# Kernel optimization log

Hardware: AMD Instinct MI355X
Metric: run time of the kernel (lower is better)

Reference implementation:

```python
import jax, jax.numpy as jnp
import numpy as np

D_MODEL = 512
DQ = D_MODEL // 4  # 128
TIME_SHIFT_START = 256
VELOCITY_START = 768
NOTE_OFF_START = 128


def conv1d(x, w, b, stride, pad):
    # x: [B, Cin, L], w: [Cout, Cin, K]
    y = jax.lax.conv_general_dilated(x, w, (stride,), [(pad, pad)],
                                     dimension_numbers=('NCH', 'OIH', 'NCH'))
    return y + b[None, :, None]


def adaptive_avg_pool1d(x, out_size):
    # faithful to torch AdaptiveAvgPool1d bin boundaries
    L = x.shape[-1]
    starts = (np.arange(out_size) * L) // out_size
    ends = np.ceil((np.arange(out_size) + 1) * L / out_size).astype(np.int64)
    cs = jnp.concatenate([jnp.zeros(x.shape[:-1] + (1,), x.dtype),
                          jnp.cumsum(x, axis=-1)], axis=-1)
    return (cs[..., ends] - cs[..., starts]) / jnp.asarray(ends - starts, x.dtype)


def setup_inputs() -> dict:
    key = jax.random.key(0)
    ks = jax.random.split(key, 20)

    def w(k, shape):
        fan_in = int(np.prod(shape[1:]))
        return jax.random.normal(k, shape, jnp.float32) / np.sqrt(fan_in)

    def b(k, n):
        return jax.random.normal(k, (n,), jnp.float32) * 0.01

    return {
        'tokens': jax.random.randint(ks[0], (32, 4096), 0, 774),
        'r1_w': w(ks[1], (32, 1, 8)),    'r1_b': b(ks[2], 32),
        'r2_w': w(ks[3], (64, 32, 4)),   'r2_b': b(ks[4], 64),
        'h1_w': w(ks[5], (64, 128, 12)), 'h1_b': b(ks[6], 64),
        'h2_w': w(ks[7], (32, 64, 8)),   'h2_b': b(ks[8], 32),
        'm1_w': w(ks[9], (64, 128, 5)),  'm1_b': b(ks[10], 64),
        'm2_w': w(ks[11], (32, 64, 3)),  'm2_b': b(ks[12], 32),
        'd1_w': w(ks[13], (16, 6, 4)),   'd1_b': b(ks[14], 16),
        'd2_w': w(ks[15], (16, 16, 3)),  'd2_b': b(ks[16], 16),
        'fc_w': w(ks[17], (D_MODEL, D_MODEL)), 'fc_b': b(ks[18], D_MODEL),
    }


def reference(tokens, r1_w, r1_b, r2_w, r2_b, h1_w, h1_b, h2_w, h2_b,
              m1_w, m1_b, m2_w, m2_b, d1_w, d1_b, d2_w, d2_b, fc_w, fc_b):
    B, S = tokens.shape
    relu = jax.nn.relu

    # rhythm: binary time-shift indicator [B,1,S]
    ts = ((tokens >= TIME_SHIFT_START) & (tokens < VELOCITY_START)).astype(jnp.float32)[:, None, :]
    r = relu(conv1d(ts, r1_w, r1_b, 2, 3))
    r = relu(conv1d(r, r2_w, r2_b, 2, 1))
    r = adaptive_avg_pool1d(r, DQ).reshape(B, -1)  # [B, 64*DQ]

    # vectorized one-hot pitch scatter (replaces the python double loop): [B,128,S]
    nm = tokens < NOTE_OFF_START
    pitch = jnp.transpose(
        jax.nn.one_hot(jnp.where(nm, tokens, 0) % 128, 128, dtype=jnp.float32)
        * nm[..., None].astype(jnp.float32), (0, 2, 1))

    h = relu(conv1d(pitch, h1_w, h1_b, 1, 6))
    h = relu(conv1d(h, h2_w, h2_b, 2, 3))
    h = adaptive_avg_pool1d(h, DQ).reshape(B, -1)  # [B, 32*DQ]

    m = relu(conv1d(pitch, m1_w, m1_b, 1, 2))
    m = relu(conv1d(m, m2_w, m2_b, 1, 1))
    m = adaptive_avg_pool1d(m, DQ).reshape(B, -1)  # [B, 32*DQ]

    # velocity one-hot scatter: [B,6,S]
    vm = tokens >= VELOCITY_START
    vel = jnp.clip(jnp.where(vm, tokens - VELOCITY_START, 0), 0, 5)
    vpat = jnp.transpose(
        jax.nn.one_hot(vel, 6, dtype=jnp.float32) * vm[..., None].astype(jnp.float32),
        (0, 2, 1))
    d = relu(conv1d(vpat, d1_w, d1_b, 1, 2))
    d = relu(conv1d(d, d2_w, d2_b, 1, 1))
    d = adaptive_avg_pool1d(d, DQ).reshape(B, -1)  # [B, 16*DQ]

    # total flattened size is 36*d_model != d_model, so torch branch always pools
    r, h, m, d = [adaptive_avg_pool1d(f[:, None, :], DQ)[:, 0] for f in (r, h, m, d)]

    combined = jnp.concatenate([r, h, m, d], axis=1)       # [B, d_model]
    feats = combined @ fc_w.T + fc_b                        # Linear
    return jnp.broadcast_to(feats[:, None, :], (B, S, D_MODEL))
```

## Files before the change

### kernel.cpp

```cpp
#include <hip/hip_runtime.h>

typedef unsigned short u16;
typedef unsigned int u32;
typedef float vf4 __attribute__((ext_vector_type(4)));
typedef unsigned int vu4 __attribute__((ext_vector_type(4)));
typedef short sh8 __attribute__((ext_vector_type(8)));
typedef float f32x4 __attribute__((ext_vector_type(4)));

__device__ __forceinline__ float bf2f(u16 u) {
  return __uint_as_float(((u32)u) << 16);
}
__device__ __forceinline__ u16 f2bf(float f) {
  u32 x = __float_as_uint(f);
  return (u16)((x + 0x7fffu + ((x >> 16) & 1u)) >> 16);
}
__device__ __forceinline__ float ldin(const void* p, int idx, int isf) {
  return isf ? ((const float*)p)[idx] : bf2f(((const u16*)p)[idx]);
}

#define OFF_FLAG  ((size_t)0)
#define OFF_WB    ((size_t)16)
#define OFF_WTH1  ((size_t)1180432)
#define OFF_WTM1  ((size_t)1573648)
#define OFF_COMB  ((size_t)1737488)
#define OFF_FEATF ((size_t)1803024)
#define OFF_FEATB ((size_t)1868560)
#define OFF_R1    ((size_t)1901328)
#define OFF_D1    ((size_t)10289936)
#define OFF_DP    ((size_t)18686736)
#define OFF_H1    ((size_t)18948880)
#define OFF_M1    ((size_t)35758864)
#define OFF_WH2B  ((size_t)52536080)
#define OFF_WH2L  ((size_t)52568848)
#define OFF_WM2B  ((size_t)52601616)
#define OFF_WM2L  ((size_t)52613904)
#define WS_NEEDED ((size_t)52626192)

#define WB_R1W 0
#define WB_R1B 256
#define WB_R2W 288
#define WB_R2B 8480
#define WB_H1B 8544
#define WB_H2W 8608
#define WB_H2B 24992
#define WB_M1B 25024
#define WB_M2W 25088
#define WB_M2B 31232
#define WB_D1W 31264
#define WB_D1B 31648
#define WB_D2W 31664
#define WB_D2B 32432
#define WB_FCW 32448
#define WB_FCB 294592
#define WB_TOTAL 295104

#define H1_STRIDE 4104
#define D1_STRIDE 4100

__global__ __launch_bounds__(256) void k_convert(
    const void* r1_w, const void* r1_b, const void* r2_w, const void* r2_b,
    const void* h1_w, const void* h1_b, const void* h2_w, const void* h2_b,
    const void* m1_w, const void* m1_b, const void* m2_w, const void* m2_b,
    const void* d1_w, const void* d1_b, const void* d2_w, const void* d2_b,
    const void* fc_w, const void* fc_b,
    int* __restrict__ flagp, float* __restrict__ wb,
    float* __restrict__ wTh1, float* __restrict__ wTm1,
    float* __restrict__ combined,
    u16* __restrict__ wh2b, u16* __restrict__ wh2l,
    u16* __restrict__ wm2b, u16* __restrict__ wm2l) {
  __shared__ int cnt[4];
  int tid = threadIdx.x;
  {
    u16 v = ((const u16*)fc_w)[2 * tid];
    int e = (v >> 7) & 0xFF;
    int outside = (e < 100 || e > 140) ? 1 : 0;
    unsigned long long m = __ballot(outside);
    if ((tid & 63) == 0) cnt[tid >> 6] = __popcll(m);
  }
  __syncthreads();
  int isf = (cnt[0] + cnt[1] + cnt[2] + cnt[3] >= 64) ? 1 : 0;
  if (blockIdx.x == 0 && tid == 0) flagp[0] = isf;

  int j = blockIdx.x * 256 + tid;
  if (j >= 473280) return;
  if (j < WB_TOTAL) {
    const void* src; int si;
    if      (j < WB_R1B) { src = r1_w; si = j; }
    else if (j < WB_R2W) { src = r1_b; si = j - WB_R1B; }
    else if (j < WB_R2B) { src = r2_w; si = j - WB_R2W; }
    else if (j < WB_H1B) { src = r2_b; si = j - WB_R2B; }
    else if (j < WB_H2W) { src = h1_b; si = j - WB_H1B; }
    else if (j < WB_H2B) { src = h2_w; si = j - WB_H2W; }
    else if (j < WB_M1B) { src = h2_b; si = j - WB_H2B; }
    else if (j < WB_M2W) { src = m1_b; si = j - WB_M1B; }
    else if (j < WB_M2B) { src = m2_w; si = j - WB_M2W; }
    else if (j < WB_D1W) { src = m2_b; si = j - WB_M2B; }
    else if (j < WB_D1B) { src = d1_w; si = j - WB_D1W; }
    else if (j < WB_D2W) { src = d1_b; si = j - WB_D1B; }
    else if (j < WB_D2B) { src = d2_w; si = j - WB_D2W; }
    else if (j < WB_FCW) { src = d2_b; si = j - WB_D2B; }
    else if (j < WB_FCB) { src = fc_w; si = j - WB_FCW; }
    else                 { src = fc_b; si = j - WB_FCB; }
    wb[j] = ldin(src, si, isf);
  } else if (j < 393408) {
    int j2 = j - WB_TOTAL;
    int o = j2 & 63, r = j2 >> 6, k = r % 12, p = r / 12;
    wTh1[j2] = ldin(h1_w, (o * 128 + p) * 12 + k, isf);
  } else if (j < 434368) {
    int j3 = j - 393408;
    int o = j3 & 63, r = j3 >> 6, k = r % 5, p = r / 5;
    wTm1[j3] = ldin(m1_w, (o * 128 + p) * 5 + k, isf);
  } else if (j < 450752) {
    combined[j - 434368] = 0.f;
  } else if (j < 467136) {
    int jj = j - 450752;
    int o = jj >> 9, rem = jj & 511, c = rem >> 3, kk = rem & 7;
    float w = ldin(h2_w, (o * 64 + c) * 8 + kk, isf);
    u16 hi = f2bf(w);
    wh2b[jj] = hi;
    wh2l[jj] = f2bf(w - bf2f(hi));
  } else {
    int jj = j - 467136;
    int o = jj / 192, rem = jj % 192, c = rem / 3, kk = rem % 3;
    float w = ldin(m2_w, (o * 64 + c) * 3 + kk, isf);
    u16 hi = f2bf(w);
    wm2b[jj] = hi;
    wm2l[jj] = f2bf(w - bf2f(hi));
  }
}


__device__ __forceinline__ void dev_r1(float* smem, const int* tok,
                                       const float* r1wf, const float* r1bf,
                                       float* r1ws, int chunk, int b) {
  float* w1s = smem;
  float* b1s = smem + 256;
  float* Ibuf = smem + 288;
  int tid = threadIdx.x;
  w1s[tid] = r1wf[tid];
  if (tid < 32) b1s[tid] = r1bf[tid];
  int t0 = chunk * 64;
  if (tid < 134) {
    int x = 2 * t0 - 3 + tid;
    float v = 0.f;
    if ((unsigned)x < 4096u) {
      int tk = tok[b * 4096 + x];
      v = (tk >= 256 && tk < 768) ? 1.f : 0.f;
    }
    Ibuf[tid] = v;
  }
  __syncthreads();
  int tl = tid & 63, og = tid >> 6;
  float iv[8];
#pragma unroll
  for (int k = 0; k < 8; ++k) iv[k] = Ibuf[2 * tl + k];
  int t = t0 + tl;
#pragma unroll
  for (int i = 0; i < 8; ++i) {
    int o = og * 8 + i;
    float acc = b1s[o];
#pragma unroll
    for (int k = 0; k < 8; ++k) acc = fmaf(w1s[o * 8 + k], iv[k], acc);
    r1ws[(size_t)(b * 32 + o) * 2048 + t] = fmaxf(acc, 0.f);
  }
}

__device__ __forceinline__ void dev_d1(float* smem, const int* tok,
                                       const float* d1wf, const float* d1bf,
                                       float* d1ws, int chunk, int b) {
  float* wds = smem;
  int* cls = (int*)(smem + 384);
  int tid = threadIdx.x;
  for (int f = tid; f < 384; f += 256) wds[f] = d1wf[f];
  int t0 = chunk * 64;
  if (tid < 67) {
    int x = t0 - 2 + tid;
    int v = -1;
    if ((unsigned)x < 4096u) {
      int tk = tok[b * 4096 + x];
      if (tk >= 768) { v = tk - 768; v = v > 5 ? 5 : v; }
    }
    cls[tid] = v;
  }
  __syncthreads();
  int tl = tid & 63, og = tid >> 6;
  int t = t0 + tl;
  if (t > 4096) return;
  int vk[4];
#pragma unroll
  for (int k = 0; k < 4; ++k) vk[k] = cls[tl + k];
#pragma unroll
  for (int i = 0; i < 4; ++i) {
    int o = og * 4 + i;
    float acc = d1bf[o];
#pragma unroll
    for (int k = 0; k < 4; ++k) {
      int v = vk[k];
      if (v >= 0) acc += wds[(o * 6 + v) * 4 + k];
    }
    d1ws[(size_t)(b * 16 + o) * D1_STRIDE + t] = fmaxf(acc, 0.f);
  }
}

__device__ __forceinline__ void dev_h1(float* smem, const int* tok,
                                       const float* wTh1, const float* h1bf,
                                       u16* h1ws, int bx, int b) {
  float (*tile)[65] = reinterpret_cast<float(*)[65]>(smem);
  int tid = threadIdx.x;
  int t0 = bx * 32;
  int o = tid & 63, sub = tid >> 6;
  float bias = h1bf[o];
#pragma unroll
  for (int j = 0; j < 8; ++j) {
    int tl = j * 4 + sub;
    int t = t0 + tl;
    float acc = bias;
    if (t <= 4096) {
#pragma unroll
      for (int k = 0; k < 12; ++k) {
        int x = t + k - 6;
        if ((unsigned)x < 4096u) {
          int p = tok[b * 4096 + x];
          if (p < 128) acc += wTh1[(p * 12 + k) * 64 + o];
        }
      }
    }
    tile[tl][o] = fmaxf(acc, 0.f);
  }
  __syncthreads();
  int o2 = tid >> 2, seg = tid & 3;
  size_t rowbase = (size_t)(b * 64 + o2) * H1_STRIDE;
  int ts = t0 + seg * 8;
  if (ts + 7 <= 4096) {
    u32 w0 = (u32)f2bf(tile[seg * 8 + 0][o2]) | ((u32)f2bf(tile[seg * 8 + 1][o2]) << 16);
    u32 w1 = (u32)f2bf(tile[seg * 8 + 2][o2]) | ((u32)f2bf(tile[seg * 8 + 3][o2]) << 16);
    u32 w2 = (u32)f2bf(tile[seg * 8 + 4][o2]) | ((u32)f2bf(tile[seg * 8 + 5][o2]) << 16);
    u32 w3 = (u32)f2bf(tile[seg * 8 + 6][o2]) | ((u32)f2bf(tile[seg * 8 + 7][o2]) << 16);
    uint4 v; v.x = w0; v.y = w1; v.z = w2; v.w = w3;
    *(uint4*)&h1ws[rowbase + ts] = v;
  } else {
    for (int i2 = 0; i2 < 8; ++i2) {
      int t = ts + i2;
      if (t <= 4096) h1ws[rowbase + t] = f2bf(tile[seg * 8 + i2][o2]);
      else if (t < H1_STRIDE) h1ws[rowbase + t] = 0;
    }
  }
}

__device__ __forceinline__ void dev_m1(float* smem, const int* tok,
                                       const float* wTm1, const float* m1bf,
                                       u16* m1ws, int bx, int b) {
  float (*tile)[65] = reinterpret_cast<float(*)[65]>(smem);
  int tid = threadIdx.x;
  int t0 = bx * 32;
  int o = tid & 63, sub = tid >> 6;
  float bias = m1bf[o];
#pragma unroll
  for (int j = 0; j < 8; ++j) {
    int tl = j * 4 + sub;
    int t = t0 + tl;
    float acc = bias;
#pragma unroll
    for (int k = 0; k < 5; ++k) {
      int x = t + k - 2;
      if ((unsigned)x < 4096u) {
        int p = tok[b * 4096 + x];
        if (p < 128) acc += wTm1[(p * 5 + k) * 64 + o];
      }
    }
    tile[tl][o] = fmaxf(acc, 0.f);
  }
  __syncthreads();
  int o2 = tid >> 2, seg = tid & 3;
  size_t rowbase = (size_t)(b * 64 + o2) * 4096;
  int ts = t0 + seg * 8;
  u32 w0 = (u32)f2bf(tile[seg * 8 + 0][o2]) | ((u32)f2bf(tile[seg * 8 + 1][o2]) << 16);
  u32 w1 = (u32)f2bf(tile[seg * 8 + 2][o2]) | ((u32)f2bf(tile[seg * 8 + 3][o2]) << 16);
  u32 w2 = (u32)f2bf(tile[seg * 8 + 4][o2]) | ((u32)f2bf(tile[seg * 8 + 5][o2]) << 16);
  u32 w3 = (u32)f2bf(tile[seg * 8 + 6][o2]) | ((u32)f2bf(tile[seg * 8 + 7][o2]) << 16);
  uint4 v; v.x = w0; v.y = w1; v.z = w2; v.w = w3;
  *(uint4*)&m1ws[rowbase + ts] = v;
}

__global__ __launch_bounds__(256) void k_cv1(const int* __restrict__ tok,
                                             const float* __restrict__ wb,
                                             const float* __restrict__ wTh1,
                                             const float* __restrict__ wTm1,
                                             float* __restrict__ r1ws,
                                             float* __restrict__ d1ws,
                                             u16* __restrict__ h1ws,
                                             u16* __restrict__ m1ws) {
  __shared__ __align__(16) float smem[2080];
  int bx = blockIdx.x;
  if (bx < 1024) {
    dev_r1(smem, tok, wb + WB_R1W, wb + WB_R1B, r1ws, bx & 31, bx >> 5);
  } else if (bx < 3104) {
    int n = bx - 1024;
    dev_d1(smem, tok, wb + WB_D1W, wb + WB_D1B, d1ws, n % 65, n / 65);
  } else if (bx < 7232) {
    int n = bx - 3104;
    dev_h1(smem, tok, wTh1, wb + WB_H1B, h1ws, n % 129, n / 129);
  } else {
    int n = bx - 7232;
    dev_m1(smem, tok, wTm1, wb + WB_M1B, m1ws, n & 127, n >> 7);
  }
}


__device__ __forceinline__ void dev_h2(const u16* h1ws,
                                       const u16* wh2b, const u16* wh2l,
                                       const float* h2bf,
                                       float* combined, int chunk, int q, int b) {
  const int tid = threadIdx.x;
  const int w = tid >> 6, l = tid & 63;
  const int quad = l >> 4, n = l & 15;
  const int ot = w & 1, tp = w >> 1;
  const int tb = q * 512 + chunk * 64;
  f32x4 acc[2];
  acc[0] = (f32x4){0.f, 0.f, 0.f, 0.f};
  acc[1] = (f32x4){0.f, 0.f, 0.f, 0.f};
  const u16* wph = wh2b + (size_t)(16 * ot + n) * 512 + quad * 8;
  const u16* wpl = wh2l + (size_t)(16 * ot + n) * 512 + quad * 8;

  for (int kc = 0; kc < 2; ++kc) {
    sh8 ah[8], al[8];
#pragma unroll
    for (int s = 0; s < 8; ++s) {
      ah[s] = *(const sh8*)(wph + kc * 256 + 32 * s);
      al[s] = *(const sh8*)(wpl + kc * 256 + 32 * s);
    }
#pragma unroll
    for (int it = 0; it < 2; ++it) {
      int t0 = tb + (2 * it + tp) * 16;
      int xbase = 2 * t0 + 2 * n - 3;
#pragma unroll
      for (int s = 0; s < 8; ++s) {
        int c = kc * 32 + 4 * s + quad;
        const u16* row = h1ws + (size_t)(b * 64 + c) * H1_STRIDE;
        sh8 bb;
        if (xbase >= 0) {
          __builtin_memcpy(&bb, row + xbase, 16);
        } else {
#pragma unroll
          for (int j = 0; j < 8; ++j) {
            int x = xbase + j;
            bb[j] = (x >= 0) ? (short)row[x] : (short)0;
          }
        }
        acc[it] = __builtin_amdgcn_mfma_f32_16x16x32_bf16(ah[s], bb, acc[it], 0, 0, 0);
        acc[it] = __builtin_amdgcn_mfma_f32_16x16x32_bf16(al[s], bb, acc[it], 0, 0, 0);
      }
    }
  }
#pragma unroll
  for (int r = 0; r < 4; ++r) {
    float bs = h2bf[16 * ot + quad * 4 + r];
    float s = fmaxf(acc[0][r] + bs, 0.f) + fmaxf(acc[1][r] + bs, 0.f);
    s += __shfl_xor(s, 1, 64);
    s += __shfl_xor(s, 2, 64);
    s += __shfl_xor(s, 4, 64);
    s += __shfl_xor(s, 8, 64);
    if (n == 0) {
      int o = 16 * ot + quad * 4 + r;
      atomicAdd(&combined[b * 512 + 128 + 4 * o + q], s * (1.f / 512.f));
    }
  }
}

__device__ __forceinline__ void dev_m2(float* smem, const u16* m1ws,
                                       const u16* wm2b, const u16* wm2l,
                                       const float* m2bf,
                                       float* combined, int sub, int q, int b) {
  u16* xs = (u16*)smem;
  const int tid = threadIdx.x;
  const int w = tid >> 6, l = tid & 63;
  const int quad = l >> 4, n = l & 15;
  const int ot = w & 1, tp = w >> 1;
  const int tb = q * 1024 + sub * 256;
  sh8 ah[6], al[6];
  {
    const u16* wph = wm2b + (size_t)(16 * ot + n) * 192 + quad * 8;
    const u16* wpl = wm2l + (size_t)(16 * ot + n) * 192 + quad * 8;
#pragma unroll
    for (int s = 0; s < 6; ++s) {
      ah[s] = *(const sh8*)(wph + 32 * s);
      al[s] = *(const sh8*)(wpl + 32 * s);
    }
  }
  float bs[4];
#pragma unroll
  for (int r = 0; r < 4; ++r) bs[r] = m2bf[16 * ot + quad * 4 + r];
  float sm[4] = {0.f, 0.f, 0.f, 0.f};
  const int gkb = quad * 8;

  for (int it = 0; it < 8; ++it) {
    for (int f = tid; f < 1280; f += 256) {
      int rg = f / 640, rem = f % 640, c = rem / 10, ch = rem % 10;
      int t0 = tb + (2 * it + rg) * 16;
      int xa = t0 - 2 + 2 * ch;
      const u16* row = m1ws + (size_t)(b * 64 + c) * 4096;
      u32 vlo = ((unsigned)xa < 4096u) ? row[xa] : 0u;
      u32 vhi = ((unsigned)(xa + 1) < 4096u) ? row[xa + 1] : 0u;
      ((u32*)xs)[f] = vlo | (vhi << 16);
    }
    __syncthreads();
    const u16* xr = xs + tp * 1280;
    f32x4 acc = {0.f, 0.f, 0.f, 0.f};
#pragma unroll
    for (int s = 0; s < 6; ++s) {
      sh8 bb;
#pragma unroll
      for (int j = 0; j < 8; ++j) {
        int gk = 32 * s + gkb + j;
        int c = (gk * 21846) >> 16;
        int kk = gk - 3 * c;
        bb[j] = (short)xr[c * 20 + n + kk + 1];
      }
      acc = __builtin_amdgcn_mfma_f32_16x16x32_bf16(ah[s], bb, acc, 0, 0, 0);
      acc = __builtin_amdgcn_mfma_f32_16x16x32_bf16(al[s], bb, acc, 0, 0, 0);
    }
#pragma unroll
    for (int r = 0; r < 4; ++r) sm[r] += fmaxf(acc[r] + bs[r], 0.f);
    __syncthreads();
  }
#pragma unroll
  for (int r = 0; r < 4; ++r) {
    float s = sm[r];
    s += __shfl_xor(s, 1, 64);
    s += __shfl_xor(s, 2, 64);
    s += __shfl_xor(s, 4, 64);
    s += __shfl_xor(s, 8, 64);
    if (n == 0) {
      int o = 16 * ot + quad * 4 + r;
      atomicAdd(&combined[b * 512 + 256 + 4 * o + q], s * (1.f / 1024.f));
    }
  }
}

__device__ __forceinline__ void dev_r2(float* smem, const float* r1ws,
                                       const float* r2wf, const float* r2bf,
                                       float* combined, int chunk, int b) {
  float* wcr = smem;
  float (*tile)[68] = reinterpret_cast<float(*)[68]>(smem + 2048);
  const int tbase = chunk * 64;
  const int half = chunk >> 3;
  const int tid = threadIdx.x;
  const int og = tid >> 6, tl = tid & 63;
  float acc[16];
#pragma unroll
  for (int i = 0; i < 16; ++i) acc[i] = 0.f;

  for (int c0 = 0; c0 < 32; c0 += 8) {
    for (int f = tid; f < 2048; f += 256) {
      int o = f & 63, r = f >> 6, k = r & 3, cc = r >> 2;
      wcr[f] = r2wf[(o * 32 + c0 + cc) * 4 + k];
    }
    for (int f = tid; f < 1056; f += 256) {
      int iu = f % 66, pc = f / 66, p = pc & 1, cc = pc >> 1;
      int x = 2 * (tbase - 1 + iu) + p;
      float v = 0.f;
      if (x >= 0 && x < 2048) v = r1ws[(size_t)(b * 32 + c0 + cc) * 2048 + x];
      tile[pc][iu] = v;
    }
    __syncthreads();
#pragma unroll
    for (int cc = 0; cc < 8; ++cc) {
      float ev[3], od[3];
#pragma unroll
      for (int f3 = 0; f3 < 3; ++f3) {
        ev[f3] = tile[cc * 2][tl + f3];
        od[f3] = tile[cc * 2 + 1][tl + f3];
      }
#pragma unroll
      for (int k = 0; k < 4; ++k) {
        const int p = (k + 1) & 1, fk = (k + 1) >> 1;
        const float* wv = &wcr[(cc * 4 + k) * 64 + og * 16];
        float4 wa = *(const float4*)wv;
        float4 wbv = *(const float4*)(wv + 4);
        float4 wcc = *(const float4*)(wv + 8);
        float4 wd = *(const float4*)(wv + 12);
        float wr[16] = {wa.x, wa.y, wa.z, wa.w, wbv.x, wbv.y, wbv.z, wbv.w,
                        wcc.x, wcc.y, wcc.z, wcc.w, wd.x, wd.y, wd.z, wd.w};
        float v0 = p ? od[fk] : ev[fk];
#pragma unroll
        for (int i = 0; i < 16; ++i) acc[i] = fmaf(v0, wr[i], acc[i]);
      }
    }
    __syncthreads();
  }
  const float inv = 1.f / 512.f;
#pragma unroll
  for (int i = 0; i < 16; ++i) {
    int o = og * 16 + i;
    float s = fmaxf(acc[i] + r2bf[o], 0.f);
#pragma unroll
    for (int d = 32; d > 0; d >>= 1) s += __shfl_down(s, d, 64);
    if (tl == 0) atomicAdd(&combined[b * 512 + 2 * o + half], s * inv);
  }
}

__device__ __forceinline__ void dev_d2(float* smem, const float* d1ws,
                                       const float* d2wf, const float* d2bf,
                                       float* dpws, int chunk, int b) {
  float* wd = smem;
  float (*dt)[132] = reinterpret_cast<float(*)[132]>(smem + 768);
  float* c2 = smem + 768 + 2112;
  const int tbase = chunk * 128;
  const int tid = threadIdx.x;
  for (int f = tid; f < 768; f += 256) wd[f] = d2wf[f];
  for (int f = tid; f < 2096; f += 256) {
    int iu = f % 131, c = f / 131;
    int x = tbase - 1 + iu;
    float v = 0.f;
    if (x >= 0 && x <= 4096) v = d1ws[(size_t)(b * 16 + c) * D1_STRIDE + x];
    dt[c][iu] = v;
  }
  __syncthreads();
  for (int idx = tid; idx < 16 * 129; idx += 256) {
    int o = idx / 129, tl = idx % 129;
    float acc = d2bf[o];
    const float* w = &wd[o * 48];
#pragma unroll 4
    for (int c = 0; c < 16; ++c) {
      acc = fmaf(dt[c][tl], w[c * 3 + 0],
            fmaf(dt[c][tl + 1], w[c * 3 + 1],
            fmaf(dt[c][tl + 2], w[c * 3 + 2], acc)));
    }
    c2[o * 133 + tl] = fmaxf(acc, 0.f);
  }
  __syncthreads();
  if (tid < 64) {
    int o = tid >> 2, qq = tid & 3;
    const float* row = c2 + o * 133 + 32 * qq;
    float s = 0.f;
#pragma unroll
    for (int j = 0; j < 33; ++j) s += row[j];
    dpws[(size_t)(b * 16 + o) * 128 + 4 * chunk + qq] = s * (1.f / 33.f);
  }
}

__global__ __launch_bounds__(256, 4) void k_cv2(const u16* __restrict__ h1ws,
                                                const u16* __restrict__ m1ws,
                                                const float* __restrict__ r1ws,
                                                const float* __restrict__ d1ws,
                                                const float* __restrict__ wb,
                                                const u16* __restrict__ wh2b,
                                                const u16* __restrict__ wh2l,
                                                const u16* __restrict__ wm2b,
                                                const u16* __restrict__ wm2l,
                                                float* __restrict__ combined,
                                                float* __restrict__ dpws) {
  __shared__ __align__(16) float smem[5008];
  int bx = blockIdx.x;
  if (bx < 1024) {
    dev_h2(h1ws, wh2b, wh2l, wb + WB_H2B, combined, bx & 7, (bx >> 3) & 3, bx >> 5);
  } else if (bx < 1536) {
    int n = bx - 1024;
    dev_m2(smem, m1ws, wm2b, wm2l, wb + WB_M2B, combined, n & 3, (n >> 2) & 3, n >> 4);
  } else if (bx < 2048) {
    int n = bx - 1536;
    dev_r2(smem, r1ws, wb + WB_R2W, wb + WB_R2B, combined, n & 15, n >> 4);
  } else {
    int n = bx - 2048;
    dev_d2(smem, d1ws, wb + WB_D2W, wb + WB_D2B, dpws, n & 31, n >> 5);
  }
}

__global__ __launch_bounds__(256) void k_fc(const float* __restrict__ combined,
                                            const float* __restrict__ dpws,
                                            const float* __restrict__ fcwf,
                                            const float* __restrict__ fcbf,
                                            float* __restrict__ featf,
                                            u16* __restrict__ featb) {
  const int b = blockIdx.x, tid = threadIdx.x;
  __shared__ float cb[512];
  cb[tid] = combined[b * 512 + tid];
  if (tid < 128) {
    cb[256 + tid] = combined[b * 512 + 256 + tid];
  } else {
    int j = tid - 128;
    int o = j >> 3, i0 = (j & 7) * 16;
    const float* row = dpws + (size_t)(b * 16 + o) * 128;
    float s = 0.f;
#pragma unroll
    for (int i = 0; i < 16; ++i) s += row[i0 + i];
    cb[384 + j] = s * (1.f / 16.f);
  }
  __syncthreads();
  for (int h = 0; h < 2; ++h) {
    int oo = h * 256 + tid;
    float acc = fcbf[oo];
    const float4* wr = (const float4*)(fcwf + (size_t)oo * 512);
#pragma unroll 8
    for (int j4 = 0; j4 < 128; ++j4) {
      float4 w = wr[j4];
      const float* c4 = &cb[j4 * 4];
      acc = fmaf(c4[0], w.x, acc);
      acc = fmaf(c4[1], w.y, acc);
      acc = fmaf(c4[2], w.z, acc);
      acc = fmaf(c4[3], w.w, acc);
    }
    featf[b * 512 + oo] = acc;
    featb[b * 512 + oo] = f2bf(acc);
  }
}

__global__ __launch_bounds__(256) void k_bcast(const int* __restrict__ flagp,
                                               const vf4* __restrict__ featf4,
                                               const vu4* __restrict__ featb4,
                                               vf4* __restrict__ outf,
                                               vu4* __restrict__ outb) {
  int base = blockIdx.x * 1024 + threadIdx.x;
  if (flagp[0]) {
#pragma unroll
    for (int s = 0; s < 4; ++s) {
      int g = base + s * 256;
      vf4 v = featf4[(g >> 19) * 128 + (g & 127)];
      __builtin_nontemporal_store(v, &outf[g]);
    }
  } else {
#pragma unroll
    for (int s = 0; s < 4; ++s) {
      int g = base + s * 256;
      if (g < 8388608) {
        vu4 v = featb4[(g >> 18) * 64 + (g & 63)];
        __builtin_nontemporal_store(v, &outb[g]);
      }
    }
  }
}

extern "C" void kernel_launch(void* const* d_in, const int* in_sizes, int n_in,
                              void* d_out, int out_size, void* d_ws, size_t ws_size,
                              hipStream_t stream) {
  if (ws_size < WS_NEEDED) return;

  const int* tokens = (const int*)d_in[0];
  const void* r1_w = d_in[1];  const void* r1_b = d_in[2];
  const void* r2_w = d_in[3];  const void* r2_b = d_in[4];
  const void* h1_w = d_in[5];  const void* h1_b = d_in[6];
  const void* h2_w = d_in[7];  const void* h2_b = d_in[8];
  const void* m1_w = d_in[9];  const void* m1_b = d_in[10];
  const void* m2_w = d_in[11]; const void* m2_b = d_in[12];
  const void* d1_w = d_in[13]; const void* d1_b = d_in[14];
  const void* d2_w = d_in[15]; const void* d2_b = d_in[16];
  const void* fc_w = d_in[17]; const void* fc_b = d_in[18];

  char* ws = (char*)d_ws;
  int*   flagp   = (int*)  (ws + OFF_FLAG);
  float* wb      = (float*)(ws + OFF_WB);
  float* wTh1    = (float*)(ws + OFF_WTH1);
  float* wTm1    = (float*)(ws + OFF_WTM1);
  float* combined= (float*)(ws + OFF_COMB);
  float* featf   = (float*)(ws + OFF_FEATF);
  u16*   featb   = (u16*)  (ws + OFF_FEATB);
  float* r1ws    = (float*)(ws + OFF_R1);
  float* d1ws    = (float*)(ws + OFF_D1);
  float* dpws    = (float*)(ws + OFF_DP);
  u16*   h1ws    = (u16*)  (ws + OFF_H1);
  u16*   m1ws    = (u16*)  (ws + OFF_M1);
  u16*   wh2b    = (u16*)  (ws + OFF_WH2B);
  u16*   wh2l    = (u16*)  (ws + OFF_WH2L);
  u16*   wm2b    = (u16*)  (ws + OFF_WM2B);
  u16*   wm2l    = (u16*)  (ws + OFF_WM2L);

  k_convert<<<1849, 256, 0, stream>>>(r1_w, r1_b, r2_w, r2_b, h1_w, h1_b, h2_w, h2_b,
                                      m1_w, m1_b, m2_w, m2_b, d1_w, d1_b, d2_w, d2_b,
                                      fc_w, fc_b, flagp, wb, wTh1, wTm1, combined,
                                      wh2b, wh2l, wm2b, wm2l);
  k_cv1<<<11328, 256, 0, stream>>>(tokens, wb, wTh1, wTm1, r1ws, d1ws, h1ws, m1ws);
  k_cv2<<<3072, 256, 0, stream>>>(h1ws, m1ws, r1ws, d1ws, wb, wh2b, wh2l, wm2b, wm2l,
                                  combined, dpws);
  k_fc<<<32, 256, 0, stream>>>(combined, dpws, wb + WB_FCW, wb + WB_FCB, featf, featb);
  k_bcast<<<16384, 256, 0, stream>>>(flagp, (const vf4*)featf, (const vu4*)featb,
                                     (vf4*)d_out, (vu4*)d_out);
}
```

Baseline: 483.5 us.

## Stage tokens in LDS, vectorize h1/m1 gathers, split FC across more blocks

The h1 and m1 first-layer convolutions now stage the block's token window in shared memory and have each thread accumulate four output channels through float4 weight loads, so redundant global token reads are removed and gather loads are vectorized. The FC kernel launches 256 blocks instead of 32, and four threads split each output's dot product and combine partials with a shuffle reduction. This raises parallelism for the small FC stage, at the cost of recomputing the combined-vector staging in every block.

```diff
diff --git a/kernel.cpp b/kernel.cpp
--- a/kernel.cpp
+++ b/kernel.cpp
@@ -206,26 +206,37 @@
                                        const float* wTh1, const float* h1bf,
                                        u16* h1ws, int bx, int b) {
   float (*tile)[65] = reinterpret_cast<float(*)[65]>(smem);
+  int* tks = (int*)(smem + 2080);
   int tid = threadIdx.x;
   int t0 = bx * 32;
-  int o = tid & 63, sub = tid >> 6;
-  float bias = h1bf[o];
-#pragma unroll
-  for (int j = 0; j < 8; ++j) {
-    int tl = j * 4 + sub;
+  const int* tokb = tok + b * 4096;
+  if (tid < 44) {
+    int x = t0 - 6 + tid;
+    tks[tid] = ((unsigned)x < 4096u) ? tokb[x] : 999;
+  }
+  __syncthreads();
+  int l = tid & 63, w = tid >> 6;
+  int og = l & 15, tr = l >> 4;
+  const float4 bias = *(const float4*)(h1bf + og * 4);
+#pragma unroll
+  for (int j = 0; j < 2; ++j) {
+    int tl = j * 16 + w * 4 + tr;
     int t = t0 + tl;
-    float acc = bias;
+    float4 acc = bias;
     if (t <= 4096) {
 #pragma unroll
       for (int k = 0; k < 12; ++k) {
-        int x = t + k - 6;
-        if ((unsigned)x < 4096u) {
-          int p = tok[b * 4096 + x];
-          if (p < 128) acc += wTh1[(p * 12 + k) * 64 + o];
+        int p = tks[tl + k];
+        if (p < 128) {
+          float4 wv = *(const float4*)(wTh1 + (p * 12 + k) * 64 + og * 4);
+          acc.x += wv.x; acc.y += wv.y; acc.z += wv.z; acc.w += wv.w;
         }
       }
     }
-    tile[tl][o] = fmaxf(acc, 0.f);
+    tile[tl][og * 4 + 0] = fmaxf(acc.x, 0.f);
+    tile[tl][og * 4 + 1] = fmaxf(acc.y, 0.f);
+    tile[tl][og * 4 + 2] = fmaxf(acc.z, 0.f);
+    tile[tl][og * 4 + 3] = fmaxf(acc.w, 0.f);
   }
   __syncthreads();
   int o2 = tid >> 2, seg = tid & 3;
@@ -251,24 +262,34 @@
                                        const float* wTm1, const float* m1bf,
                                        u16* m1ws, int bx, int b) {
   float (*tile)[65] = reinterpret_cast<float(*)[65]>(smem);
+  int* tks = (int*)(smem + 2080);
   int tid = threadIdx.x;
   int t0 = bx * 32;
-  int o = tid & 63, sub = tid >> 6;
-  float bias = m1bf[o];
-#pragma unroll
-  for (int j = 0; j < 8; ++j) {
-    int tl = j * 4 + sub;
-    int t = t0 + tl;
-    float acc = bias;
+  const int* tokb = tok + b * 4096;
+  if (tid < 36) {
+    int x = t0 - 2 + tid;
+    tks[tid] = ((unsigned)x < 4096u) ? tokb[x] : 999;
+  }
+  __syncthreads();
+  int l = tid & 63, w = tid >> 6;
+  int og = l & 15, tr = l >> 4;
+  const float4 bias = *(const float4*)(m1bf + og * 4);
+#pragma unroll
+  for (int j = 0; j < 2; ++j) {
+    int tl = j * 16 + w * 4 + tr;
+    float4 acc = bias;
 #pragma unroll
     for (int k = 0; k < 5; ++k) {
-      int x = t + k - 2;
-      if ((unsigned)x < 4096u) {
-        int p = tok[b * 4096 + x];
-        if (p < 128) acc += wTm1[(p * 5 + k) * 64 + o];
+      int p = tks[tl + k];
+      if (p < 128) {
+        float4 wv = *(const float4*)(wTm1 + (p * 5 + k) * 64 + og * 4);
+        acc.x += wv.x; acc.y += wv.y; acc.z += wv.z; acc.w += wv.w;
       }
     }
-    tile[tl][o] = fmaxf(acc, 0.f);
+    tile[tl][og * 4 + 0] = fmaxf(acc.x, 0.f);
+    tile[tl][og * 4 + 1] = fmaxf(acc.y, 0.f);
+    tile[tl][og * 4 + 2] = fmaxf(acc.z, 0.f);
+    tile[tl][og * 4 + 3] = fmaxf(acc.w, 0.f);
   }
   __syncthreads();
   int o2 = tid >> 2, seg = tid & 3;
@@ -290,7 +311,7 @@
                                              float* __restrict__ d1ws,
                                              u16* __restrict__ h1ws,
                                              u16* __restrict__ m1ws) {
-  __shared__ __align__(16) float smem[2080];
+  __shared__ __align__(16) float smem[2128];
   int bx = blockIdx.x;
   if (bx < 1024) {
     dev_r1(smem, tok, wb + WB_R1W, wb + WB_R1B, r1ws, bx & 31, bx >> 5);
@@ -572,7 +593,9 @@
                                             const float* __restrict__ fcbf,
                                             float* __restrict__ featf,
                                             u16* __restrict__ featb) {
-  const int b = blockIdx.x, tid = threadIdx.x;
+  const int bx = blockIdx.x;
+  const int b = bx >> 3, oct = bx & 7;
+  const int tid = threadIdx.x;
   __shared__ float cb[512];
   cb[tid] = combined[b * 512 + tid];
   if (tid < 128) {
@@ -587,21 +610,24 @@
     cb[384 + j] = s * (1.f / 16.f);
   }
   __syncthreads();
-  for (int h = 0; h < 2; ++h) {
-    int oo = h * 256 + tid;
-    float acc = fcbf[oo];
-    const float4* wr = (const float4*)(fcwf + (size_t)oo * 512);
+  const int oo = oct * 64 + (tid >> 2), part = tid & 3;
+  float acc = 0.f;
+  const float4* wr = (const float4*)(fcwf + (size_t)oo * 512 + part * 128);
 #pragma unroll 8
-    for (int j4 = 0; j4 < 128; ++j4) {
-      float4 w = wr[j4];
-      const float* c4 = &cb[j4 * 4];
-      acc = fmaf(c4[0], w.x, acc);
-      acc = fmaf(c4[1], w.y, acc);
-      acc = fmaf(c4[2], w.z, acc);
-      acc = fmaf(c4[3], w.w, acc);
-    }
-    featf[b * 512 + oo] = acc;
-    featb[b * 512 + oo] = f2bf(acc);
+  for (int j4 = 0; j4 < 32; ++j4) {
+    float4 w = wr[j4];
+    const float* c4 = &cb[part * 128 + j4 * 4];
+    acc = fmaf(c4[0], w.x, acc);
+    acc = fmaf(c4[1], w.y, acc);
+    acc = fmaf(c4[2], w.z, acc);
+    acc = fmaf(c4[3], w.w, acc);
+  }
+  acc += __shfl_xor(acc, 1, 64);
+  acc += __shfl_xor(acc, 2, 64);
+  if (part == 0) {
+    float r = acc + fcbf[oo];
+    featf[b * 512 + oo] = r;
+    featb[b * 512 + oo] = f2bf(r);
   }
 }
 
@@ -671,7 +697,7 @@
   k_cv1<<<11328, 256, 0, stream>>>(tokens, wb, wTh1, wTm1, r1ws, d1ws, h1ws, m1ws);
   k_cv2<<<3072, 256, 0, stream>>>(h1ws, m1ws, r1ws, d1ws, wb, wh2b, wh2l, wm2b, wm2l,
                                   combined, dpws);
-  k_fc<<<32, 256, 0, stream>>>(combined, dpws, wb + WB_FCW, wb + WB_FCB, featf, featb);
+  k_fc<<<256, 256, 0, stream>>>(combined, dpws, wb + WB_FCW, wb + WB_FCB, featf, featb);
   k_bcast<<<16384, 256, 0, stream>>>(flagp, (const vf4*)featf, (const vu4*)featb,
                                      (vf4*)d_out, (vu4*)d_out);
 }
```

Result: faster. 424.1 us (-12.3%).
